# Kernel optimization log

Hardware: AMD Instinct MI355X
Metric: run time of the kernel (lower is better)

Reference implementation:

```python
import jax, jax.numpy as jnp
import numpy as np

CODEBOOK_SIZE = 8192
EMBED_DIM = 512
COMMITMENT_COST = 0.25
B, N = 16, 2048


def setup_inputs() -> dict:
    key = jax.random.key(0)
    kz, kc = jax.random.split(key)
    z = jax.random.normal(kz, (B, N, EMBED_DIM), dtype=jnp.float32)
    # torch init: uniform(-1/K, 1/K)
    scale = 1.0 / CODEBOOK_SIZE
    codebook = jax.random.uniform(kc, (CODEBOOK_SIZE, EMBED_DIM), dtype=jnp.float32,
                                  minval=-scale, maxval=scale)
    return {"z": z, "codebook": codebook}


def reference(z, codebook):
    Bd, Nd, D = z.shape
    flat_z = z.reshape(-1, D)  # (B*N, D)
    # squared L2 distances via expansion: ||z||^2 + ||e||^2 - 2 z.e
    distances = (jnp.sum(flat_z * flat_z, axis=1, keepdims=True)
                 + jnp.sum(codebook * codebook, axis=1)
                 - 2.0 * flat_z @ codebook.T)  # (B*N, K)
    indices = jnp.argmin(distances, axis=1)  # (B*N,)
    quantized = codebook[indices].reshape(Bd, Nd, D)
    # mse_loss default reduction='mean'
    codebook_loss = jnp.mean((jax.lax.stop_gradient(quantized) - z) ** 2)
    commitment_loss = jnp.mean((quantized - jax.lax.stop_gradient(z)) ** 2)
    vq_loss = codebook_loss + COMMITMENT_COST * commitment_loss
    # straight-through estimator
    quantized = z + jax.lax.stop_gradient(quantized - z)
    return quantized, indices.reshape(Bd, Nd), vq_loss
```

## Files before the change

kernel.cpp:

```cpp
#include <hip/hip_runtime.h>

#define M_ROWS 32768
#define DIM    512
#define KCB    8192
#define BM     128
#define BN     128
#define NSLAB  128

typedef int    i32x4  __attribute__((ext_vector_type(4)));
typedef unsigned u32;
typedef unsigned long long u64;

#define AS1(p) ((const __attribute__((address_space(1))) void*)(p))
#define AS3(p) ((__attribute__((address_space(3))) void*)(p))

__global__ void __launch_bounds__(256)
vq_pack_all(const float* __restrict__ z, const float* __restrict__ cb,
            unsigned char* __restrict__ zfrag, unsigned char* __restrict__ efrag,
            float* __restrict__ A) {
    int b = (int)blockIdx.x;
    if (b < M_ROWS / 4) {
        int w = threadIdx.x >> 6, j = threadIdx.x & 63;
        int row = b * 4 + w;
        const float* zr = z + (size_t)row * DIM + j * 8;
        float4 v0 = *(const float4*)zr;
        float4 v1 = *(const float4*)(zr + 4);

        float s = v0.x*v0.x + v0.y*v0.y + v0.z*v0.z + v0.w*v0.w
                + v1.x*v1.x + v1.y*v1.y + v1.z*v1.z + v1.w*v1.w;
        #pragma unroll
        for (int off = 32; off > 0; off >>= 1) s += __shfl_down(s, off, 64);
        if (j == 0) A[row] = s;

        int b0 = __float2int_rn(v0.x * 16.0f);
        int b1 = __float2int_rn(v0.y * 16.0f);
        int b2 = __float2int_rn(v0.z * 16.0f);
        int b3 = __float2int_rn(v0.w * 16.0f);
        int b4 = __float2int_rn(v1.x * 16.0f);
        int b5 = __float2int_rn(v1.y * 16.0f);
        int b6 = __float2int_rn(v1.z * 16.0f);
        int b7 = __float2int_rn(v1.w * 16.0f);
        int2 p;
        p.x = (b0 & 255) | ((b1 & 255) << 8) | ((b2 & 255) << 16) | ((b3 & 255) << 24);
        p.y = (b4 & 255) | ((b5 & 255) << 8) | ((b6 & 255) << 16) | ((b7 & 255) << 24);

        int rb  = row >> 7;
        int g   = (row >> 4) & 7;
        int sdx = j >> 3;
        int lhi = (j >> 1) & 3;
        int l   = (lhi << 4) | (row & 15);
        int u   = (rb << 12) | (sdx << 9) | (g << 6) | l;
        *(int2*)(zfrag + ((size_t)u << 4) + ((j & 1) << 3)) = p;
    } else {
        int u = (b - M_ROWS / 4) * 256 + (int)threadIdx.x;
        int l  = u & 63;
        int g  = (u >> 6) & 7;
        int s  = (u >> 9) & 7;
        int rb = u >> 12;
        int row = rb * 128 + g * 16 + (l & 15);
        int k   = s * 64 + (l >> 4) * 16;
        const float* src = cb + (size_t)row * DIM + k;
        const float scale = 8192.0f * 127.0f;
        int dw[4];
        #pragma unroll
        for (int d4 = 0; d4 < 4; ++d4) {
            float4 v = *(const float4*)(src + d4 * 4);
            int c0 = __float2int_rn(v.x * scale);
            int c1 = __float2int_rn(v.y * scale);
            int c2 = __float2int_rn(v.z * scale);
            int c3 = __float2int_rn(v.w * scale);
            dw[d4] = (c0 & 255) | ((c1 & 255) << 8) | ((c2 & 255) << 16)
                   | ((c3 & 255) << 24);
        }
        i32x4 o = { dw[0], dw[1], dw[2], dw[3] };
        *(i32x4*)(efrag + (size_t)u * 16) = o;
    }
}

__global__ void __launch_bounds__(256, 4)
vq_gemm(const unsigned char* __restrict__ zf, const unsigned char* __restrict__ ef,
        const float* __restrict__ Anorm, u32* __restrict__ cand) {
    extern __shared__ char lds[];
    const int tid  = threadIdx.x;
    const int lane = tid & 63;
    const int wid  = tid >> 6;
    const int wm   = wid >> 1;
    const int wn   = wid & 1;
    const int bid0 = (int)blockIdx.x;
    const int xcd  = bid0 & 7;
    const int loc  = bid0 >> 3;
    const int cbk  = loc >> 5;
    const int rb   = (xcd << 5) | (loc & 31);
    const char* zsrc = (const char*)zf + ((size_t)rb  << 16);
    const char* esrc = (const char*)ef + ((size_t)cbk << 16);
    const char* ebase = esrc + ((size_t)((wn << 2)) << 10) + ((size_t)lane << 4);

    i32x4 acc[4][4];
    #pragma unroll
    for (int m = 0; m < 4; ++m)
        #pragma unroll
        for (int n = 0; n < 4; ++n) acc[m][n] = (i32x4)0;

#define STAGE(t) do {                                                         \
    char* dst_ = lds + (((t) & 1) << 13);                                     \
    _Pragma("unroll")                                                         \
    for (int j = 0; j < 2; ++j) {                                             \
        int n2 = (wid << 1) | j;                     \
        const char* src_ = zsrc + (((t) << 13) + (n2 << 10)) + (lane << 4);   \
        __builtin_amdgcn_global_load_lds(AS1(src_), AS3(dst_ + (n2 << 10)), 16, 0, 0); \
    }                                                                         \
} while (0)

#define COMPUTE(t) do {                                                       \
    const char* bufA_ = lds + (((t) & 1) << 13);                              \
    const char* eb_ = ebase + ((t) << 13);                                    \
    i32x4 b0 = *(const i32x4*)(eb_);                                          \
    i32x4 b1 = *(const i32x4*)(eb_ + 1024);                                   \
    i32x4 b2 = *(const i32x4*)(eb_ + 2048);                                   \
    i32x4 b3 = *(const i32x4*)(eb_ + 3072);                                   \
    i32x4 af[4];                                                              \
    _Pragma("unroll")                                                         \
    for (int m = 0; m < 4; ++m)                                               \
        af[m] = *(const i32x4*)(bufA_ + (((wm << 2) | m) << 10) + (lane << 4)); \
    __builtin_amdgcn_s_setprio(1);                                            \
    _Pragma("unroll")                                                         \
    for (int m = 0; m < 4; ++m) {                                             \
        acc[m][0] = __builtin_amdgcn_mfma_i32_16x16x64_i8(af[m], b0, acc[m][0], 0, 0, 0); \
        acc[m][1] = __builtin_amdgcn_mfma_i32_16x16x64_i8(af[m], b1, acc[m][1], 0, 0, 0); \
    }                                                                         \
    _Pragma("unroll")                                                         \
    for (int m = 0; m < 4; ++m) {                                             \
        acc[m][2] = __builtin_amdgcn_mfma_i32_16x16x64_i8(af[m], b2, acc[m][2], 0, 0, 0); \
        acc[m][3] = __builtin_amdgcn_mfma_i32_16x16x64_i8(af[m], b3, acc[m][3], 0, 0, 0); \
    }                                                                         \
    __builtin_amdgcn_s_setprio(0);                                            \
} while (0)

#define STEP2(t) do {                                                         \
    STAGE((t) + 1);                                                           \
    COMPUTE(t);                                                               \
    __syncthreads();                                                          \
} while (0)

    STAGE(0);
    __syncthreads();
    STEP2(0); STEP2(1); STEP2(2); STEP2(3); STEP2(4); STEP2(5); STEP2(6);
    COMPUTE(7);
    __syncthreads();

    const float INV = 2.0f / (16.0f * 8192.0f * 127.0f);
    float* As = (float*)lds;
    if (tid < BM) As[tid] = Anorm[rb * BM + tid];
    __syncthreads();

    const u32 colbase = (u32)((cbk << 7) + (wn << 6) + (lane & 15));
    #pragma unroll
    for (int m = 0; m < 4; ++m) {
        #pragma unroll
        for (int rg = 0; rg < 4; ++rg) {
            int row_l = (wm << 6) + (m << 4) + ((lane >> 4) << 2) + rg;
            float Arow = As[row_l];
            u32 abase = __float_as_uint(Arow) - 8192u;
            u32 k1 = 0xFFFFFFFFu, k2 = 0xFFFFFFFFu;
            #pragma unroll
            for (int nj = 0; nj < 4; ++nj) {
                float t = (float)acc[m][nj][rg] * INV;
                float d = Arow - t;
                u32 io = __float_as_uint(d) - abase;
                io = io > 65535u ? 65535u : io;
                u32 key = io * 8192u + (colbase + (u32)(nj << 4));
                u32 mx = key > k1 ? key : k1;
                k1 = key < k1 ? key : k1;
                k2 = mx < k2 ? mx : k2;
            }
            #pragma unroll
            for (int mk = 1; mk < 16; mk <<= 1) {
                u32 o1 = (u32)__shfl_xor((int)k1, mk);
                u32 o2 = (u32)__shfl_xor((int)k2, mk);
                u32 lo = k1 < o1 ? k1 : o1;
                u32 hi = k1 < o1 ? o1 : k1;
                u32 so = k2 < o2 ? k2 : o2;
                k1 = lo;
                k2 = hi < so ? hi : so;
            }
            if ((lane & 15) == 0) {
                size_t base = (size_t)(rb * BM + row_l) * (2 * NSLAB)
                            + (size_t)(((cbk << 1) | wn) << 1);
                cand[base]     = k1;
                cand[base + 1] = k2;
            }
        }
    }
}

__global__ void __launch_bounds__(256)
vq_refine_gather(const float* __restrict__ z, const float* __restrict__ cb,
                 const float* __restrict__ Anorm, const u32* __restrict__ cand,
                 float* __restrict__ outQ, float* __restrict__ outIdx,
                 double* __restrict__ lossRow) {
    __shared__ float zs[4][DIM];
    __shared__ int   sc[4][128];
    int w = threadIdx.x >> 6, lane = threadIdx.x & 63;
    int row = blockIdx.x * 4 + w;

    const float* zr = z + (size_t)row * DIM;
    *(float4*)&zs[w][lane * 4]       = *(const float4*)(zr + lane * 4);
    *(float4*)&zs[w][256 + lane * 4] = *(const float4*)(zr + 256 + lane * 4);

    const u32* cr = cand + (size_t)row * (2 * NSLAB);
    i32x4 cv = *(const i32x4*)(cr + lane * 4);
    u32 c[4] = { (u32)cv[0], (u32)cv[1], (u32)cv[2], (u32)cv[3] };
    u32 mn = c[0];
    #pragma unroll
    for (int k = 1; k < 4; ++k) if (c[k] < mn) mn = c[k];
    #pragma unroll
    for (int m = 32; m > 0; m >>= 1) {
        u32 o = (u32)__shfl_xor((int)mn, m);
        if (o < mn) mn = o;
    }
    float Arow = Anorm[row];
    u32 abase = __float_as_uint(Arow) - 8192u;
    float minD = __uint_as_float(abase + (mn >> 13));
    float thr = minD + 2e-3f;
    u64 below = ((u64)1 << lane) - 1;
    int base = 0;
    #pragma unroll
    for (int k = 0; k < 4; ++k) {
        bool sk = __uint_as_float(abase + (c[k] >> 13)) <= thr;
        u64 mk = __ballot(sk);
        if (sk) {
            int slot = base + __popcll(mk & below);
            if (slot < 128) sc[w][slot] = (int)(c[k] & 8191u);
        }
        base += __popcll(mk);
    }
    int ns = base < 128 ? base : 128;
    __syncthreads();

    float4 zv0 = *(const float4*)&zs[w][lane * 8];
    float4 zv1 = *(const float4*)&zs[w][lane * 8 + 4];
    u64 best = ~0ull;
    for (int j = 0; j < ns; ++j) {
        int col = sc[w][j];
        const float* e = cb + (size_t)col * DIM + lane * 8;
        float4 ev0 = *(const float4*)e;
        float4 ev1 = *(const float4*)(e + 4);
        float p = zv0.x * ev0.x;
        p = fmaf(zv0.y, ev0.y, p);
        p = fmaf(zv0.z, ev0.z, p);
        p = fmaf(zv0.w, ev0.w, p);
        p = fmaf(zv1.x, ev1.x, p);
        p = fmaf(zv1.y, ev1.y, p);
        p = fmaf(zv1.z, ev1.z, p);
        p = fmaf(zv1.w, ev1.w, p);
        #pragma unroll
        for (int off = 32; off > 0; off >>= 1) p += __shfl_xor(p, off);
        float d = Arow - 2.0f * p;
        u64 pk = ((u64)__float_as_uint(d) << 32) | (u32)col;
        if (pk < best) best = pk;
    }
    int bi = (int)(u32)best;

    const float* q = cb + (size_t)bi * DIM;
    float* o = outQ + (size_t)row * DIM;
    double ls = 0.0;
    #pragma unroll
    for (int j = 0; j < 2; ++j) {
        int off = j * 256 + lane * 4;
        float4 qv = *(const float4*)(q + off);
        float4 zv = *(const float4*)&zs[w][off];
        float t0 = qv.x - zv.x, t1 = qv.y - zv.y;
        float t2 = qv.z - zv.z, t3 = qv.w - zv.w;
        float4 ov = { zv.x + t0, zv.y + t1, zv.z + t2, zv.w + t3 };
        *(float4*)(o + off) = ov;
        ls += (double)t0 * t0 + (double)t1 * t1
            + (double)t2 * t2 + (double)t3 * t3;
    }
    #pragma unroll
    for (int off = 32; off > 0; off >>= 1) ls += __shfl_down(ls, off, 64);
    if (lane == 0) { lossRow[row] = ls; outIdx[row] = (float)bi; }
}

__global__ void __launch_bounds__(256)
vq_loss_final(const double* __restrict__ lossRow, float* __restrict__ outLoss) {
    __shared__ double sm[256];
    double s = 0.0;
    for (int i = threadIdx.x; i < M_ROWS; i += 256) s += lossRow[i];
    sm[threadIdx.x] = s;
    __syncthreads();
    for (int st = 128; st > 0; st >>= 1) {
        if (threadIdx.x < st) sm[threadIdx.x] += sm[threadIdx.x + st];
        __syncthreads();
    }
    if (threadIdx.x == 0)
        outLoss[0] = (float)(1.25 * sm[0] / (double)((size_t)M_ROWS * DIM));
}

extern "C" void kernel_launch(void* const* d_in, const int* in_sizes, int n_in,
                              void* d_out, int out_size, void* d_ws, size_t ws_size,
                              hipStream_t stream) {
    const float* z  = (const float*)d_in[0];
    const float* cb = (const float*)d_in[1];

    float* out     = (float*)d_out;
    float* outQ    = out;
    float* outIdx  = out + (size_t)M_ROWS * DIM;
    float* outLoss = out + (size_t)M_ROWS * DIM + M_ROWS;

    unsigned char* zfrag = (unsigned char*)d_out;

    char* ws = (char*)d_ws;
    float*  A       = (float*)ws;            ws += (size_t)M_ROWS * 4;
    double* lossRow = (double*)ws;           ws += (size_t)M_ROWS * 8;
    unsigned char* efrag = (unsigned char*)ws; ws += (size_t)KCB * DIM;
    u32*    cand    = (u32*)ws;

    hipLaunchKernelGGL(vq_pack_all, dim3(M_ROWS / 4 + KCB * DIM / 16 / 256),
                       dim3(256), 0, stream, z, cb, zfrag, efrag, A);
    hipLaunchKernelGGL(vq_gemm, dim3((M_ROWS / BM) * (KCB / BN)), dim3(256),
                       16384, stream, zfrag, efrag, A, cand);
    hipLaunchKernelGGL(vq_refine_gather, dim3(M_ROWS / 4), dim3(256), 0, stream,
                       z, cb, A, cand, outQ, outIdx, lossRow);
    hipLaunchKernelGGL(vq_loss_final, dim3(1), dim3(256), 0, stream, lossRow, outLoss);
}
```

Before: 349.2 us.

## Load GEMM A fragments directly from global memory instead of LDS staging

Measured after the change: 344.0 us. About the same (-1.5%).

```diff
diff --git a/kernel.cpp b/kernel.cpp
--- a/kernel.cpp
+++ b/kernel.cpp
@@ -10,9 +10,6 @@
 typedef int    i32x4  __attribute__((ext_vector_type(4)));
 typedef unsigned u32;
 typedef unsigned long long u64;
-
-#define AS1(p) ((const __attribute__((address_space(1))) void*)(p))
-#define AS3(p) ((__attribute__((address_space(3))) void*)(p))
 
 __global__ void __launch_bounds__(256)
 vq_pack_all(const float* __restrict__ z, const float* __restrict__ cb,
@@ -80,7 +77,7 @@
 __global__ void __launch_bounds__(256, 4)
 vq_gemm(const unsigned char* __restrict__ zf, const unsigned char* __restrict__ ef,
         const float* __restrict__ Anorm, u32* __restrict__ cand) {
-    extern __shared__ char lds[];
+    __shared__ float As[BM];
     const int tid  = threadIdx.x;
     const int lane = tid & 63;
     const int wid  = tid >> 6;
@@ -93,7 +90,8 @@
     const int rb   = (xcd << 5) | (loc & 31);
     const char* zsrc = (const char*)zf + ((size_t)rb  << 16);
     const char* esrc = (const char*)ef + ((size_t)cbk << 16);
-    const char* ebase = esrc + ((size_t)((wn << 2)) << 10) + ((size_t)lane << 4);
+    const char* abase_p = zsrc + ((size_t)(wm << 2) << 10) + ((size_t)lane << 4);
+    const char* ebase_p = esrc + ((size_t)(wn << 2) << 10) + ((size_t)lane << 4);
 
     i32x4 acc[4][4];
     #pragma unroll
@@ -101,55 +99,41 @@
         #pragma unroll
         for (int n = 0; n < 4; ++n) acc[m][n] = (i32x4)0;
 
-#define STAGE(t) do {                                                         \
-    char* dst_ = lds + (((t) & 1) << 13);                                     \
-    _Pragma("unroll")                                                         \
-    for (int j = 0; j < 2; ++j) {                                             \
-        int n2 = (wid << 1) | j;                     \
-        const char* src_ = zsrc + (((t) << 13) + (n2 << 10)) + (lane << 4);   \
-        __builtin_amdgcn_global_load_lds(AS1(src_), AS3(dst_ + (n2 << 10)), 16, 0, 0); \
-    }                                                                         \
-} while (0)
-
 #define COMPUTE(t) do {                                                       \
-    const char* bufA_ = lds + (((t) & 1) << 13);                              \
-    const char* eb_ = ebase + ((t) << 13);                                    \
+    const char* ab_ = abase_p + ((t) << 13);                                  \
+    const char* eb_ = ebase_p + ((t) << 13);                                  \
+    i32x4 a0 = *(const i32x4*)(ab_);                                          \
+    i32x4 a1 = *(const i32x4*)(ab_ + 1024);                                   \
+    i32x4 a2 = *(const i32x4*)(ab_ + 2048);                                   \
+    i32x4 a3 = *(const i32x4*)(ab_ + 3072);                                   \
     i32x4 b0 = *(const i32x4*)(eb_);                                          \
     i32x4 b1 = *(const i32x4*)(eb_ + 1024);                                   \
     i32x4 b2 = *(const i32x4*)(eb_ + 2048);                                   \
     i32x4 b3 = *(const i32x4*)(eb_ + 3072);                                   \
-    i32x4 af[4];                                                              \
-    _Pragma("unroll")                                                         \
-    for (int m = 0; m < 4; ++m)                                               \
-        af[m] = *(const i32x4*)(bufA_ + (((wm << 2) | m) << 10) + (lane << 4)); \
     __builtin_amdgcn_s_setprio(1);                                            \
-    _Pragma("unroll")                                                         \
-    for (int m = 0; m < 4; ++m) {                                             \
-        acc[m][0] = __builtin_amdgcn_mfma_i32_16x16x64_i8(af[m], b0, acc[m][0], 0, 0, 0); \
-        acc[m][1] = __builtin_amdgcn_mfma_i32_16x16x64_i8(af[m], b1, acc[m][1], 0, 0, 0); \
-    }                                                                         \
-    _Pragma("unroll")                                                         \
-    for (int m = 0; m < 4; ++m) {                                             \
-        acc[m][2] = __builtin_amdgcn_mfma_i32_16x16x64_i8(af[m], b2, acc[m][2], 0, 0, 0); \
-        acc[m][3] = __builtin_amdgcn_mfma_i32_16x16x64_i8(af[m], b3, acc[m][3], 0, 0, 0); \
-    }                                                                         \
+    acc[0][0] = __builtin_amdgcn_mfma_i32_16x16x64_i8(a0, b0, acc[0][0], 0, 0, 0); \
+    acc[0][1] = __builtin_amdgcn_mfma_i32_16x16x64_i8(a0, b1, acc[0][1], 0, 0, 0); \
+    acc[1][0] = __builtin_amdgcn_mfma_i32_16x16x64_i8(a1, b0, acc[1][0], 0, 0, 0); \
+    acc[1][1] = __builtin_amdgcn_mfma_i32_16x16x64_i8(a1, b1, acc[1][1], 0, 0, 0); \
+    acc[2][0] = __builtin_amdgcn_mfma_i32_16x16x64_i8(a2, b0, acc[2][0], 0, 0, 0); \
+    acc[2][1] = __builtin_amdgcn_mfma_i32_16x16x64_i8(a2, b1, acc[2][1], 0, 0, 0); \
+    acc[3][0] = __builtin_amdgcn_mfma_i32_16x16x64_i8(a3, b0, acc[3][0], 0, 0, 0); \
+    acc[3][1] = __builtin_amdgcn_mfma_i32_16x16x64_i8(a3, b1, acc[3][1], 0, 0, 0); \
+    acc[0][2] = __builtin_amdgcn_mfma_i32_16x16x64_i8(a0, b2, acc[0][2], 0, 0, 0); \
+    acc[0][3] = __builtin_amdgcn_mfma_i32_16x16x64_i8(a0, b3, acc[0][3], 0, 0, 0); \
+    acc[1][2] = __builtin_amdgcn_mfma_i32_16x16x64_i8(a1, b2, acc[1][2], 0, 0, 0); \
+    acc[1][3] = __builtin_amdgcn_mfma_i32_16x16x64_i8(a1, b3, acc[1][3], 0, 0, 0); \
+    acc[2][2] = __builtin_amdgcn_mfma_i32_16x16x64_i8(a2, b2, acc[2][2], 0, 0, 0); \
+    acc[2][3] = __builtin_amdgcn_mfma_i32_16x16x64_i8(a2, b3, acc[2][3], 0, 0, 0); \
+    acc[3][2] = __builtin_amdgcn_mfma_i32_16x16x64_i8(a3, b2, acc[3][2], 0, 0, 0); \
+    acc[3][3] = __builtin_amdgcn_mfma_i32_16x16x64_i8(a3, b3, acc[3][3], 0, 0, 0); \
     __builtin_amdgcn_s_setprio(0);                                            \
 } while (0)
 
-#define STEP2(t) do {                                                         \
-    STAGE((t) + 1);                                                           \
-    COMPUTE(t);                                                               \
-    __syncthreads();                                                          \
-} while (0)
-
-    STAGE(0);
-    __syncthreads();
-    STEP2(0); STEP2(1); STEP2(2); STEP2(3); STEP2(4); STEP2(5); STEP2(6);
-    COMPUTE(7);
-    __syncthreads();
+    COMPUTE(0); COMPUTE(1); COMPUTE(2); COMPUTE(3);
+    COMPUTE(4); COMPUTE(5); COMPUTE(6); COMPUTE(7);
 
     const float INV = 2.0f / (16.0f * 8192.0f * 127.0f);
-    float* As = (float*)lds;
     if (tid < BM) As[tid] = Anorm[rb * BM + tid];
     __syncthreads();
 
@@ -318,7 +302,7 @@
     hipLaunchKernelGGL(vq_pack_all, dim3(M_ROWS / 4 + KCB * DIM / 16 / 256),
                        dim3(256), 0, stream, z, cb, zfrag, efrag, A);
     hipLaunchKernelGGL(vq_gemm, dim3((M_ROWS / BM) * (KCB / BN)), dim3(256),
-                       16384, stream, zfrag, efrag, A, cand);
+                       0, stream, zfrag, efrag, A, cand);
     hipLaunchKernelGGL(vq_refine_gather, dim3(M_ROWS / 4), dim3(256), 0, stream,
                        z, cb, A, cand, outQ, outIdx, lossRow);
     hipLaunchKernelGGL(vq_loss_final, dim3(1), dim3(256), 0, stream, lossRow, outLoss);
```
